# Kernel optimization log

Measured on AMD Instinct MI355X. Metric: run time of the kernel, lower is better.

The kernel has to match this reference:

```python
import jax, jax.numpy as jnp
import numpy as np

B, T, F, M = 32, 256, 512, 4   # batch, pred_len (=d_model=state_size), feature_dim (=mamba seq), time-mark feats
N = F - M                      # number of variates in x_enc
T2 = 2 * T
EPS = 1e-5


def setup_inputs() -> dict:
    key = jax.random.key(0)
    it = iter(jax.random.split(key, 32))
    def nrm(*s):
        return jax.random.normal(next(it), s, jnp.float32) * 0.02
    inp = {
        "x_enc": jax.random.normal(next(it), (B, T, N), jnp.float32),
        "x_mark_enc": jax.random.normal(next(it), (B, T, M), jnp.float32),
        "x_dec": jnp.zeros((1, 1, 1), jnp.float32),
        "x_mark_dec": jnp.zeros((1, 1, 1), jnp.float32),
        # 3 structurally identical MambaBlocks -> stack params on leading dim 3
        "norm_w": jnp.ones((3, T), jnp.float32),
        "inp_W": nrm(3, T, T2), "inp_b": jnp.zeros((3, T2), jnp.float32),
        "conv_W": nrm(3, F, F, 3), "conv_b": jnp.zeros((3, F), jnp.float32),
        "convlin_W": nrm(3, T2, T2), "convlin_b": jnp.zeros((3, T2), jnp.float32),
        "fc1_W": nrm(3, T2, T2), "fc1_b": jnp.zeros((3, T2), jnp.float32),
        "fc2_W": nrm(3, T2, T), "fc2_b": jnp.zeros((3, T), jnp.float32),
        "fc3_W": nrm(3, T2, T), "fc3_b": jnp.zeros((3, T), jnp.float32),
        "D_W": nrm(3, T, T2), "D_b": jnp.zeros((3, T2), jnp.float32),
        "out_W": nrm(3, T2, T), "out_b": jnp.ones((3, T), jnp.float32),  # out_proj.bias init to 1.0
        "proj_W": nrm(T, T), "proj_b": jnp.zeros((T,), jnp.float32),
    }
    return inp


def _rmsnorm(x, w):
    return x * jax.lax.rsqrt(jnp.mean(x * x, -1, keepdims=True) + EPS) * w


def _conv1d(x, W, b):
    # x: [B, C, L], W: [C_out, C_in, 3], padding=1
    y = jax.lax.conv_general_dilated(x, W, (1,), [(1, 1)], dimension_numbers=("NCH", "OIH", "NCH"))
    return y + b[None, :, None]


def _s6(x, fc1W, fc1b, fc2W, fc2b, fc3W, fc3b):
    # h is zero-initialized each call, so dA=exp(delta*A) multiplies zeros and
    # y = einsum('bln,bldn->bld', C, x[...,None]*dB) = delta * x * <C,B>_n
    Bmat = x @ fc2W + fc2b                         # [B, L, n]
    Cmat = x @ fc3W + fc3b                         # [B, L, n]
    delta = jax.nn.softplus(x @ fc1W + fc1b)       # [B, L, d]
    cb = jnp.einsum("bln,bln->bl", Cmat, Bmat)   # contraction over state dim
    return delta * x * cb[:, :, None]


def _block(x, i, p):
    xn = _rmsnorm(x, p["norm_w"][i])
    xp = xn @ p["inp_W"][i] + p["inp_b"][i]                      # [B, F, 2T]
    xc = jax.nn.silu(_conv1d(xp, p["conv_W"][i], p["conv_b"][i]))
    xco = xc @ p["convlin_W"][i] + p["convlin_b"][i]
    xssm = _s6(xco, p["fc1_W"][i], p["fc1_b"][i], p["fc2_W"][i], p["fc2_b"][i], p["fc3_W"][i], p["fc3_b"][i])
    xres = jax.nn.silu(xn @ p["D_W"][i] + p["D_b"][i])
    return (jax.nn.silu(xssm) * xres) @ p["out_W"][i] + p["out_b"][i]


def _forward(x_enc, x_mark_enc, p):
    means = jax.lax.stop_gradient(jnp.mean(x_enc, 1, keepdims=True))  # detached in torch
    xe = x_enc - means
    stdev = jnp.sqrt(jnp.var(xe, axis=1, keepdims=True) + 1e-5)       # NOT detached in torch
    xe = xe / stdev
    x = jnp.concatenate([xe, x_mark_enc], axis=2).transpose(0, 2, 1)  # [B, F, T]
    for i in range(3):
        x = _block(x, i, p)
    dec = (x @ p["proj_W"] + p["proj_b"]).transpose(0, 2, 1)          # [B, T, F]
    return dec[:, :, :N] * stdev + means                              # pred_len == T


def reference(x_enc, x_mark_enc, x_dec, x_mark_dec, norm_w, inp_W, inp_b, conv_W, conv_b, convlin_W, convlin_b, fc1_W, fc1_b, fc2_W, fc2_b, fc3_W, fc3_b, D_W, D_b, out_W, out_b, proj_W, proj_b):
    p = dict(norm_w=norm_w, inp_W=inp_W, inp_b=inp_b, conv_W=conv_W, conv_b=conv_b, convlin_W=convlin_W, convlin_b=convlin_b, fc1_W=fc1_W, fc1_b=fc1_b, fc2_W=fc2_W, fc2_b=fc2_b, fc3_W=fc3_W, fc3_b=fc3_b, D_W=D_W, D_b=D_b, out_W=out_W, out_b=out_b, proj_W=proj_W, proj_b=proj_b)
    return _forward(x_enc, x_mark_enc, p)
```

## Files before the change

### kernel.cpp

```cpp
#include <hip/hip_runtime.h>
#include <hip/hip_bf16.h>
#include <math.h>

typedef __hip_bfloat16 bf16;
typedef short short8 __attribute__((ext_vector_type(8)));
typedef short short4v __attribute__((ext_vector_type(4)));
typedef float floatx4 __attribute__((ext_vector_type(4)));

constexpr int CB_ = 32;
constexpr int CT = 256;
constexpr int CF = 512;
constexpr int CN = 508;
constexpr int CM = 4;
constexpr int CT2 = 512;
constexpr int MROWS = CB_ * CF;
constexpr int PADL = 528;

__device__ __forceinline__ float b2f(bf16 v) { return __bfloat162float(v); }
__device__ __forceinline__ bf16 f2b(float v) { return __float2bfloat16(v); }
__device__ __forceinline__ float s2f(short s) {
    unsigned u = ((unsigned)(unsigned short)s) << 16;
    return __builtin_bit_cast(float, u);
}
__device__ __forceinline__ short f2s(float v) {
    bf16 t = __float2bfloat16(v);
    return __builtin_bit_cast(short, t);
}
__device__ __forceinline__ float silu_f(float x) { return x / (1.0f + __expf(-x)); }
__device__ __forceinline__ float softplus_f(float x) {
    return fmaxf(x, 0.0f) + __logf(1.0f + __expf(-fabsf(x)));
}

__device__ __forceinline__ void gl_lds16(const bf16* g, short* l) {
    __builtin_amdgcn_global_load_lds(
        (const __attribute__((address_space(1))) unsigned int*)(g),
        (__attribute__((address_space(3))) unsigned int*)(l), 16, 0, 0);
}


constexpr int CONV3 = 3 * 512 * 512;
constexpr int MTILES = 3520;
struct P8 { const float* s[8]; bf16* d[8]; };
__global__ __launch_bounds__(256) void prepack_all_kernel(P8 p, const float* __restrict__ nw,
                                                          const float* __restrict__ convW,
                                                          bf16* __restrict__ convD,
                                                          bf16* __restrict__ xpT,
                                                          float* __restrict__ CBv) {
    int bid = blockIdx.x;
    if (bid >= MTILES) {
        int idx = (bid - MTILES) * 256 + threadIdx.x;
        if (idx < CONV3) {
            int ci = idx & 511;
            int co = (idx >> 9) & 511;
            int ib = idx >> 18;
            const float* src = convW + ((size_t)(ib * 512 + co) * 512 + ci) * 3;
            #pragma unroll
            for (int t = 0; t < 3; t++)
                convD[(((size_t)(ib * 3 + t) * 512 + co) << 9) + ci] = f2b(src[t]);
        } else if (idx < CONV3 + 32768) {
            int j = idx - CONV3;
            int ci = j & 511;
            int w = (j >> 9) & 1;
            int b = j >> 10;
            xpT[((size_t)b * PADL + (w ? 513 : 0)) * 512 + ci] = f2b(0.0f);
        } else if (idx < CONV3 + 32768 + MROWS) {
            CBv[idx - CONV3 - 32768] = 0.0f;
        }
        return;
    }
    const int Ks[8]   = {256, 256, 512, 512, 512, 512, 512, 256};
    const int Ns[8]   = {512, 512, 512, 256, 256, 512, 256, 256};
    const int zs[8]   = {3, 3, 3, 3, 3, 3, 3, 1};
    const int dstr[8] = {262144, 262144, 524288, 524288, 524288, 262144, 131072, 65536};
    const int rml[8]  = {1, 1, 1, 2, 2, 1, 1, 1};
    const int rad[8]  = {0, 0, 0, 0, 1, 0, 0, 0};
    int m = 0, acc = 0;
    for (m = 0; m < 8; m++) {
        int c = (Ns[m] >> 5) * (Ks[m] >> 5) * zs[m];
        if (bid < acc + c) break;
        acc += c;
    }
    int lid = bid - acc;
    int K = Ks[m], N = Ns[m];
    int tx = N >> 5, ty = K >> 5;
    int z = lid / (tx * ty), rem = lid % (tx * ty);
    int k0 = (rem / tx) * 32, n0 = (rem % tx) * 32;
    const float* s = p.s[m] + (size_t)z * K * N;
    bf16* d = p.d[m] + (size_t)z * dstr[m];
    int mul = rml[m], add = rad[m];
    bool fold = (m <= 1);
    __shared__ float Ts[32][33];
    for (int e = threadIdx.x; e < 1024; e += 256) {
        int r = e >> 5, c = e & 31;
        float v = s[(size_t)(k0 + r) * N + n0 + c];
        if (fold) v *= nw[z * 256 + k0 + r];
        Ts[r][c] = v;
    }
    __syncthreads();
    for (int e = threadIdx.x; e < 1024; e += 256) {
        int r = e >> 5, c = e & 31;
        d[(size_t)((n0 + r) * mul + add) * K + k0 + c] = f2b(Ts[c][r]);
    }
}

__global__ __launch_bounds__(256) void buildx_kernel(
    const float* __restrict__ xe, const float* __restrict__ xm,
    float* __restrict__ means, float* __restrict__ stdev,
    bf16* __restrict__ X0, float* __restrict__ SCL) {
    __shared__ float L[256][65];
    __shared__ float red_s[4][64], red_q[4][64];
    __shared__ float stat_m[64], stat_i[64];
    int blk = blockIdx.x;
    int b = blk >> 3, f0 = (blk & 7) * 64;
    int tid = threadIdx.x;
    int j = tid & 63, tq = tid >> 6;
    int f = f0 + j;
    float ps = 0.f, pq = 0.f;
    const float* xep = xe + (size_t)b * CT * CN + f;
    const float* xmp = xm + (size_t)b * CT * CM + (f - CN);
    #pragma unroll 4
    for (int tt = 0; tt < 64; tt++) {
        int t = tq * 64 + tt;
        float v = (f < CN) ? xep[(size_t)t * CN] : xmp[(size_t)t * CM];
        L[t][j] = v;
        ps += v;
        pq += v * v;
    }
    red_s[tq][j] = ps;
    red_q[tq][j] = pq;
    __syncthreads();
    if (tid < 64) {
        int ff = f0 + tid;
        float s = red_s[0][tid] + red_s[1][tid] + red_s[2][tid] + red_s[3][tid];
        float q = red_q[0][tid] + red_q[1][tid] + red_q[2][tid] + red_q[3][tid];
        float mean, isd, msq;
        if (ff < CN) {
            mean = s * (1.0f / 256.0f);
            float var = fmaxf(q * (1.0f / 256.0f) - mean * mean, 0.0f);
            float sd = sqrtf(var + 1e-5f);
            isd = 1.0f / sd;
            means[b * CN + ff] = mean;
            stdev[b * CN + ff] = sd;
            msq = var / (var + 1e-5f);
        } else {
            mean = 0.0f;
            isd = 1.0f;
            msq = q * (1.0f / 256.0f);
        }
        stat_m[tid] = mean;
        stat_i[tid] = isd;
        SCL[b * 512 + ff] = rsqrtf(msq + 1e-5f);
    }
    __syncthreads();
    bf16* outp = X0 + ((size_t)(b * 512 + f0)) * 256;
    int t = tid;
    #pragma unroll 4
    for (int fp = 0; fp < 64; fp++) {
        float val = (L[t][fp] - stat_m[fp]) * stat_i[fp];
        outp[(size_t)fp * 256 + t] = f2b(val);
    }
}

template <int EPI>
__global__ __launch_bounds__(256) void g64_kernel(const bf16* __restrict__ A,
                                                  const bf16* __restrict__ Wt,
                                                  int K,
                                                  const float* __restrict__ b1,
                                                  const float* __restrict__ b2,
                                                  const float* __restrict__ SCL,
                                                  const float* __restrict__ CBin,
                                                  float* __restrict__ CBout,
                                                  bf16* __restrict__ o1,
                                                  bf16* __restrict__ o2,
                                                  int Ncols,
                                                  const float* __restrict__ means,
                                                  const float* __restrict__ stdev,
                                                  float* __restrict__ outf) {
    __shared__ __align__(16) short As[128 * 64];
    __shared__ __align__(16) short Bs[64 * 64];
    const int tid = threadIdx.x;
    const int lane = tid & 63;
    const int wave = tid >> 6;
    const int m0 = blockIdx.x * 128, n0 = blockIdx.y * 64;

    const int lrow8 = lane >> 3;
    const int lcolS = (((lane & 7) ^ lrow8) << 3);
    const int wm = (wave & 1) * 64, wn = (wave >> 1) * 32;
    const int fr = lane & 15, quad = lane >> 4;
    const int fr7 = fr & 7;

    floatx4 acc[4][2];
    #pragma unroll
    for (int i = 0; i < 4; i++)
        #pragma unroll
        for (int j = 0; j < 2; j++) acc[i][j] = (floatx4){0.f, 0.f, 0.f, 0.f};

    for (int k0 = 0; k0 < K; k0 += 64) {
        for (int ca = wave; ca < 16; ca += 4)
            gl_lds16(A + (size_t)(m0 + ca * 8 + lrow8) * K + k0 + lcolS, &As[ca * 512]);
        for (int cb = wave; cb < 8; cb += 4)
            gl_lds16(Wt + (size_t)(n0 + cb * 8 + lrow8) * K + k0 + lcolS, &Bs[cb * 512]);
        __syncthreads();
        #pragma unroll
        for (int s = 0; s < 2; s++) {
            const int co = (((s * 4 + quad) ^ fr7) << 3);
            short8 af[4], bfv[2];
            #pragma unroll
            for (int i = 0; i < 4; i++) af[i] = *(const short8*)&As[(wm + i * 16 + fr) * 64 + co];
            #pragma unroll
            for (int j = 0; j < 2; j++) bfv[j] = *(const short8*)&Bs[(wn + j * 16 + fr) * 64 + co];
            #pragma unroll
            for (int i = 0; i < 4; i++)
                #pragma unroll
                for (int j = 0; j < 2; j++)
                    acc[i][j] = __builtin_amdgcn_mfma_f32_16x16x32_bf16(af[i], bfv[j], acc[i][j], 0, 0, 0);
        }
        __syncthreads();
    }

    if (EPI == 0) {
        #pragma unroll
        for (int j = 0; j < 2; j++) {
            int n = n0 + wn + j * 16 + fr;
            float bv = b1[n];
            #pragma unroll
            for (int i = 0; i < 4; i++) {
                int mb = m0 + wm + i * 16 + quad * 4;
                #pragma unroll
                for (int r = 0; r < 4; r++)
                    o1[(size_t)(mb + r) * Ncols + n] = f2b(acc[i][j][r] + bv);
            }
        }
    } else if (EPI == 3) {
        #pragma unroll
        for (int j = 0; j < 2; j++) {
            int t = n0 + wn + j * 16 + fr;
            float bv = b1[t];
            #pragma unroll
            for (int i = 0; i < 4; i++) {
                int mb = m0 + wm + i * 16 + quad * 4;
                int b = mb >> 9;
                int nv = mb & 511;
                if (nv < CN) {
                    floatx4 o;
                    #pragma unroll
                    for (int r = 0; r < 4; r++) {
                        int sn = b * CN + nv + r;
                        o[r] = (acc[i][j][r] + bv) * stdev[sn] + means[sn];
                    }
                    *(floatx4*)(outf + ((size_t)(b * CT + t)) * CN + nv) = o;
                }
            }
        }
    } else if (EPI == 4) {
        if (n0 < 512) {
            int b = (m0 + wm) >> 9;
            #pragma unroll
            for (int i = 0; i < 4; i++) {
                int mb = m0 + wm + i * 16 + quad * 4;
                float sclr[4];
                #pragma unroll
                for (int r = 0; r < 4; r++) sclr[r] = SCL[mb + r];
                int ci = mb & 511;
                #pragma unroll
                for (int j = 0; j < 2; j++) {
                    int n = n0 + wn + j * 16 + fr;
                    float bv = b1[n];
                    bf16* dst = o1 + ((size_t)b * PADL + n + 1) * 512;
                    short4v pk;
                    #pragma unroll
                    for (int r = 0; r < 4; r++) pk[r] = f2s(acc[i][j][r] * sclr[r] + bv);
                    *(short4v*)(dst + ci) = pk;
                }
            }
        } else {
            #pragma unroll
            for (int i = 0; i < 4; i++) {
                int mb = m0 + wm + i * 16 + quad * 4;
                float sclr[4];
                #pragma unroll
                for (int r = 0; r < 4; r++) sclr[r] = SCL[mb + r];
                #pragma unroll
                for (int j = 0; j < 2; j++) {
                    int n = n0 + wn + j * 16 + fr;
                    float bv = b2[n - 512];
                    #pragma unroll
                    for (int r = 0; r < 4; r++)
                        o2[(size_t)(mb + r) * 512 + (n - 512)] =
                            f2b(silu_f(acc[i][j][r] * sclr[r] + bv));
                }
            }
        }
    } else if (EPI == 5) {
        if (n0 < 512) {
            #pragma unroll
            for (int i = 0; i < 4; i++) {
                int mb = m0 + wm + i * 16 + quad * 4;
                #pragma unroll
                for (int j = 0; j < 2; j++) {
                    int n = n0 + wn + j * 16 + fr;
                    float bv = b1[n];
                    #pragma unroll
                    for (int r = 0; r < 4; r++) {
                        size_t off = (size_t)(mb + r) * 512 + n;
                        float delta = softplus_f(acc[i][j][r] + bv);
                        outf[off] = delta * b2f(A[off]);
                    }
                }
            }
        } else {
            float bv[2];
            #pragma unroll
            for (int j = 0; j < 2; j++) {
                int nn = n0 + wn + j * 16 + fr - 512;
                int c = nn >> 1;
                bv[j] = (fr & 1) ? CBin[c] : b2[c];
            }
            #pragma unroll
            for (int i = 0; i < 4; i++) {
                #pragma unroll
                for (int r = 0; r < 4; r++) {
                    float s = 0.f;
                    #pragma unroll
                    for (int j = 0; j < 2; j++) {
                        float v = acc[i][j][r] + bv[j];
                        s += v * __shfl_xor(v, 1);
                    }
                    s += __shfl_xor(s, 2);
                    s += __shfl_xor(s, 4);
                    s += __shfl_xor(s, 8);
                    if (fr == 0)
                        atomicAdd(&CBout[m0 + wm + i * 16 + quad * 4 + r], s * 0.5f);
                }
            }
        }
    }
}

__global__ __launch_bounds__(256) void conv_mfma_kernel(const bf16* __restrict__ Wc,
                                                        const bf16* __restrict__ xpT,
                                                        const float* __restrict__ bias,
                                                        bf16* __restrict__ Out,
                                                        float* __restrict__ CBvZ) {
    __shared__ __align__(16) short As[3 * 64 * 64];
    __shared__ __align__(16) short Bs[72 * 64];
    const int tid = threadIdx.x;
    const int lane = tid & 63;
    const int wave = tid >> 6;
    int bx = blockIdx.x;
    if (bx < 128 && tid < 128) CBvZ[bx * 128 + tid] = 0.0f;
    int b = bx >> 6, rem = bx & 63;
    int mt = rem >> 3, nt = rem & 7;
    const int m0 = mt * 64, n0 = nt * 64;
    const bf16* xb = xpT + (size_t)b * PADL * 512;

    const int lrow8 = lane >> 3;
    const int lcolS = (((lane & 7) ^ lrow8) << 3);
    const int wm = (wave & 1) * 32, wn = (wave >> 1) * 32;
    const int fr = lane & 15, quad = lane >> 4;
    const int fr7 = fr & 7;

    floatx4 acc[2][2];
    #pragma unroll
    for (int i = 0; i < 2; i++)
        #pragma unroll
        for (int j = 0; j < 2; j++) acc[i][j] = (floatx4){0.f, 0.f, 0.f, 0.f};

    for (int k0 = 0; k0 < 512; k0 += 64) {
        for (int ga = wave; ga < 24; ga += 4) {
            int tap = ga >> 3, rg = ga & 7;
            gl_lds16(Wc + (size_t)tap * 262144 + (size_t)(m0 + rg * 8 + lrow8) * 512 + k0 + lcolS,
                     &As[tap * 4096 + rg * 512]);
        }
        for (int gb = wave; gb < 9; gb += 4) {
            gl_lds16(xb + (size_t)(n0 + gb * 8 + lrow8) * 512 + k0 + lcolS, &Bs[gb * 512]);
        }
        __syncthreads();
        #pragma unroll
        for (int s = 0; s < 2; s++) {
            const int sq = s * 4 + quad;
            #pragma unroll
            for (int tap = 0; tap < 3; tap++) {
                const int coA = ((sq ^ fr7) << 3);
                const int coB = ((sq ^ ((fr + tap) & 7)) << 3);
                short8 af[2], bfv[2];
                #pragma unroll
                for (int i = 0; i < 2; i++)
                    af[i] = *(const short8*)&As[tap * 4096 + (wm + i * 16 + fr) * 64 + coA];
                #pragma unroll
                for (int j = 0; j < 2; j++)
                    bfv[j] = *(const short8*)&Bs[(wn + j * 16 + fr + tap) * 64 + coB];
                #pragma unroll
                for (int i = 0; i < 2; i++)
                    #pragma unroll
                    for (int j = 0; j < 2; j++)
                        acc[i][j] = __builtin_amdgcn_mfma_f32_16x16x32_bf16(af[i], bfv[j], acc[i][j], 0, 0, 0);
            }
        }
        __syncthreads();
    }
    bf16* ob = Out + (size_t)b * CF * CT2;
    #pragma unroll
    for (int i = 0; i < 2; i++) {
        int mb = m0 + wm + i * 16 + quad * 4;
        #pragma unroll
        for (int r = 0; r < 4; r++) {
            float bv = bias[mb + r];
            #pragma unroll
            for (int j = 0; j < 2; j++) {
                int n = n0 + wn + j * 16 + fr;
                ob[(size_t)(mb + r) * CT2 + n] = f2b(silu_f(acc[i][j][r] + bv));
            }
        }
    }
}

__global__ __launch_bounds__(256) void gemm_scl_gate_kernel(const float* __restrict__ P,
                                                            const bf16* __restrict__ Xres,
                                                            const float* __restrict__ CBv,
                                                            const bf16* __restrict__ Wt,
                                                            const float* __restrict__ bias,
                                                            bf16* __restrict__ Xo,
                                                            float* __restrict__ SCL) {
    __shared__ __align__(16) short As[32 * 64];
    __shared__ __align__(16) short Bs[256 * 64];
    __shared__ float red[4][32];
    const int tid = threadIdx.x;
    const int lane = tid & 63;
    const int wave = tid >> 6;
    const int m0 = blockIdx.x * 32;

    const int lrow8 = lane >> 3;
    const int lcolS = (((lane & 7) ^ lrow8) << 3);
    const int wn = wave * 64;
    const int fr = lane & 15, quad = lane >> 4;
    const int fr7 = fr & 7;

    floatx4 acc[2][4];
    #pragma unroll
    for (int i = 0; i < 2; i++)
        #pragma unroll
        for (int j = 0; j < 4; j++) acc[i][j] = (floatx4){0.f, 0.f, 0.f, 0.f};

    const int arow = m0 + wave * 8 + lrow8;
    const float cbr = CBv[arow];

    for (int k0 = 0; k0 < 512; k0 += 64) {
        for (int c = wave; c < 32; c += 4)
            gl_lds16(Wt + (size_t)(c * 8 + lrow8) * 512 + k0 + lcolS, &Bs[c * 512]);
        {
            int col = k0 + lcolS;
            const float* pp = P + (size_t)arow * 512 + col;
            floatx4 p0 = *(const floatx4*)pp;
            floatx4 p1 = *(const floatx4*)(pp + 4);
            short8 xr = *(const short8*)(Xres + (size_t)arow * 512 + col);
            short8 g;
            #pragma unroll
            for (int e = 0; e < 4; e++) {
                g[e] = f2s(silu_f(p0[e] * cbr) * s2f(xr[e]));
                g[4 + e] = f2s(silu_f(p1[e] * cbr) * s2f(xr[4 + e]));
            }
            *(short8*)&As[wave * 512 + lrow8 * 64 + (lane & 7) * 8] = g;
        }
        __syncthreads();
        #pragma unroll
        for (int s = 0; s < 2; s++) {
            const int co = (((s * 4 + quad) ^ fr7) << 3);
            short8 af[2], bfv[4];
            #pragma unroll
            for (int i = 0; i < 2; i++) af[i] = *(const short8*)&As[(i * 16 + fr) * 64 + co];
            #pragma unroll
            for (int j = 0; j < 4; j++) bfv[j] = *(const short8*)&Bs[(wn + j * 16 + fr) * 64 + co];
            #pragma unroll
            for (int i = 0; i < 2; i++)
                #pragma unroll
                for (int j = 0; j < 4; j++)
                    acc[i][j] = __builtin_amdgcn_mfma_f32_16x16x32_bf16(af[i], bfv[j], acc[i][j], 0, 0, 0);
        }
        __syncthreads();
    }
    #pragma unroll
    for (int j = 0; j < 4; j++) {
        float bv = bias[wn + j * 16 + fr];
        #pragma unroll
        for (int i = 0; i < 2; i++)
            #pragma unroll
            for (int r = 0; r < 4; r++) acc[i][j][r] += bv;
    }
    #pragma unroll
    for (int i = 0; i < 2; i++) {
        #pragma unroll
        for (int r = 0; r < 4; r++) {
            float s = 0.f;
            #pragma unroll
            for (int j = 0; j < 4; j++) s += acc[i][j][r] * acc[i][j][r];
            #pragma unroll
            for (int o = 8; o > 0; o >>= 1) s += __shfl_xor(s, o);
            if (fr == 0) red[wave][i * 16 + quad * 4 + r] = s;
        }
    }
    __syncthreads();
    if (tid < 32) {
        float tot = red[0][tid] + red[1][tid] + red[2][tid] + red[3][tid];
        SCL[m0 + tid] = rsqrtf(tot * (1.0f / CT) + 1e-5f);
    }
    #pragma unroll
    for (int j = 0; j < 4; j++) {
        int n = wn + j * 16 + fr;
        #pragma unroll
        for (int i = 0; i < 2; i++) {
            int rl = i * 16 + quad * 4;
            #pragma unroll
            for (int r = 0; r < 4; r++)
                Xo[(size_t)(m0 + rl + r) * CT + n] = f2b(acc[i][j][r]);
        }
    }
}

extern "C" void kernel_launch(void* const* d_in, const int* in_sizes, int n_in,
                              void* d_out, int out_size, void* d_ws, size_t ws_size,
                              hipStream_t stream) {
    const float* x_enc  = (const float*)d_in[0];
    const float* x_mark = (const float*)d_in[1];
    const float* norm_w = (const float*)d_in[4];
    const float* inp_W  = (const float*)d_in[5];
    const float* inp_b  = (const float*)d_in[6];
    const float* conv_W = (const float*)d_in[7];
    const float* conv_b = (const float*)d_in[8];
    const float* convlin_W = (const float*)d_in[9];
    const float* convlin_b = (const float*)d_in[10];
    const float* fc1_W = (const float*)d_in[11];
    const float* fc1_b = (const float*)d_in[12];
    const float* fc2_W = (const float*)d_in[13];
    const float* fc2_b = (const float*)d_in[14];
    const float* fc3_W = (const float*)d_in[15];
    const float* fc3_b = (const float*)d_in[16];
    const float* D_W   = (const float*)d_in[17];
    const float* D_b   = (const float*)d_in[18];
    const float* out_W = (const float*)d_in[19];
    const float* out_b = (const float*)d_in[20];
    const float* proj_W = (const float*)d_in[21];
    const float* proj_b = (const float*)d_in[22];

    char* ws = (char*)d_ws;
    float* MEANS = (float*)(ws);
    float* STDEV = (float*)(ws + 65536);
    float* CBv   = (float*)(ws + 131072);
    float* SCL   = (float*)(ws + 196608);
    bf16* wt = (bf16*)(ws + 262144);
    bf16* wt_g1      = wt;
    bf16* wt_g3      = wt + 786432;
    bf16* wt_convlin = wt + 2359296;
    bf16* wt_out     = wt + 3145728;
    bf16* wt_proj    = wt + 3538944;
    bf16* wt_conv    = wt + 3604480;
    bf16* xpT = (bf16*)(ws + 12189696);
    const size_t POOLB = 16777216;
    bf16* X    = (bf16*)(ws + 29491200);
    bf16* XRES = (bf16*)(ws + 29491200 + POOLB);
    bf16* XC   = (bf16*)(ws + 29491200 + 2 * POOLB);
    bf16* XCO  = (bf16*)(ws + 29491200 + 3 * POOLB);
    float* Pf  = (float*)(ws + 29491200 + 4 * POOLB);
    float* out = (float*)d_out;

    P8 p;
    p.s[0] = inp_W;  p.d[0] = wt_g1;
    p.s[1] = D_W;    p.d[1] = wt_g1 + 131072;
    p.s[2] = fc1_W;  p.d[2] = wt_g3;
    p.s[3] = fc2_W;  p.d[3] = wt_g3 + 262144;
    p.s[4] = fc3_W;  p.d[4] = wt_g3 + 262144;
    p.s[5] = convlin_W; p.d[5] = wt_convlin;
    p.s[6] = out_W;  p.d[6] = wt_out;
    p.s[7] = proj_W; p.d[7] = wt_proj;
    int tailBlocks = (CONV3 + 32768 + MROWS + 255) / 256;
    prepack_all_kernel<<<MTILES + tailBlocks, 256, 0, stream>>>(
        p, norm_w, conv_W, wt_conv, xpT, CBv);

    buildx_kernel<<<256, 256, 0, stream>>>(x_enc, x_mark, MEANS, STDEV, X, SCL);

    for (int i = 0; i < 3; i++) {
        g64_kernel<4><<<dim3(128, 16), 256, 0, stream>>>(
            X, wt_g1 + (size_t)i * 262144, 256, inp_b + i * CT2, D_b + i * CT2, SCL,
            nullptr, nullptr, xpT, XRES, 1024, nullptr, nullptr, nullptr);
        conv_mfma_kernel<<<2048, 256, 0, stream>>>(wt_conv + (size_t)i * 786432, xpT,
                                                   conv_b + i * CF, XC, CBv);
        g64_kernel<0><<<dim3(128, 8), 256, 0, stream>>>(
            XC, wt_convlin + (size_t)i * 262144, 512, convlin_b + i * CT2, nullptr, nullptr,
            nullptr, nullptr, XCO, nullptr, 512, nullptr, nullptr, nullptr);
        g64_kernel<5><<<dim3(128, 16), 256, 0, stream>>>(
            XCO, wt_g3 + (size_t)i * 524288, 512, fc1_b + i * CT2, fc2_b + i * CT, nullptr,
            fc3_b + i * CT, CBv, nullptr, nullptr, 0, nullptr, nullptr, Pf);
        gemm_scl_gate_kernel<<<512, 256, 0, stream>>>(
            Pf, XRES, CBv, wt_out + (size_t)i * 131072, out_b + i * CT, X, SCL);
    }

    g64_kernel<3><<<dim3(128, 4), 256, 0, stream>>>(
        X, wt_proj, 256, proj_b, nullptr, nullptr, nullptr, nullptr, nullptr,
        nullptr, 0, MEANS, STDEV, out);
}
```

Before: 514.4 us.

## Store delta*x in bf16, split gate GEMM over N with atomic sum-of-squares

The fc1 epilogue now writes delta*x as bf16 instead of fp32, halving that intermediate's traffic. The gated out-projection GEMM is split into two column halves to double its block count. Because a block no longer sees a full row, the RMS statistic is accumulated as a sum of squares with atomicAdd, and consumers compute rsqrt on the fly. The SSQ buffer is zeroed inside the fc1 kernel, which adds atomics, a cross-kernel ordering dependency and an extra bf16 rounding of the intermediate.

```diff
diff --git a/kernel.cpp b/kernel.cpp
--- a/kernel.cpp
+++ b/kernel.cpp
@@ -106,7 +106,7 @@
 __global__ __launch_bounds__(256) void buildx_kernel(
     const float* __restrict__ xe, const float* __restrict__ xm,
     float* __restrict__ means, float* __restrict__ stdev,
-    bf16* __restrict__ X0, float* __restrict__ SCL) {
+    bf16* __restrict__ X0, float* __restrict__ SSQ) {
     __shared__ float L[256][65];
     __shared__ float red_s[4][64], red_q[4][64];
     __shared__ float stat_m[64], stat_i[64];
@@ -149,7 +149,7 @@
         }
         stat_m[tid] = mean;
         stat_i[tid] = isd;
-        SCL[b * 512 + ff] = rsqrtf(msq + 1e-5f);
+        SSQ[b * 512 + ff] = msq * 256.0f;
     }
     __syncthreads();
     bf16* outp = X0 + ((size_t)(b * 512 + f0)) * 256;
@@ -167,7 +167,7 @@
                                                   int K,
                                                   const float* __restrict__ b1,
                                                   const float* __restrict__ b2,
-                                                  const float* __restrict__ SCL,
+                                                  const float* __restrict__ SSQ,
                                                   const float* __restrict__ CBin,
                                                   float* __restrict__ CBout,
                                                   bf16* __restrict__ o1,
@@ -183,6 +183,8 @@
     const int wave = tid >> 6;
     const int m0 = blockIdx.x * 128, n0 = blockIdx.y * 64;
 
+    if (EPI == 5 && blockIdx.y == 0 && tid < 128) outf[blockIdx.x * 128 + tid] = 0.0f;
+
     const int lrow8 = lane >> 3;
     const int lcolS = (((lane & 7) ^ lrow8) << 3);
     const int wm = (wave & 1) * 64, wn = (wave >> 1) * 32;
@@ -260,7 +262,8 @@
                 int mb = m0 + wm + i * 16 + quad * 4;
                 float sclr[4];
                 #pragma unroll
-                for (int r = 0; r < 4; r++) sclr[r] = SCL[mb + r];
+                for (int r = 0; r < 4; r++)
+                    sclr[r] = rsqrtf(SSQ[mb + r] * (1.0f / 256.0f) + 1e-5f);
                 int ci = mb & 511;
                 #pragma unroll
                 for (int j = 0; j < 2; j++) {
@@ -279,7 +282,8 @@
                 int mb = m0 + wm + i * 16 + quad * 4;
                 float sclr[4];
                 #pragma unroll
-                for (int r = 0; r < 4; r++) sclr[r] = SCL[mb + r];
+                for (int r = 0; r < 4; r++)
+                    sclr[r] = rsqrtf(SSQ[mb + r] * (1.0f / 256.0f) + 1e-5f);
                 #pragma unroll
                 for (int j = 0; j < 2; j++) {
                     int n = n0 + wn + j * 16 + fr;
@@ -304,7 +308,7 @@
                     for (int r = 0; r < 4; r++) {
                         size_t off = (size_t)(mb + r) * 512 + n;
                         float delta = softplus_f(acc[i][j][r] + bv);
-                        outf[off] = delta * b2f(A[off]);
+                        o1[off] = f2b(delta * b2f(A[off]));
                     }
                 }
             }
@@ -415,73 +419,68 @@
     }
 }
 
-__global__ __launch_bounds__(256) void gemm_scl_gate_kernel(const float* __restrict__ P,
+__global__ __launch_bounds__(256) void gemm_scl_gate_kernel(const bf16* __restrict__ P,
                                                             const bf16* __restrict__ Xres,
                                                             const float* __restrict__ CBv,
                                                             const bf16* __restrict__ Wt,
                                                             const float* __restrict__ bias,
                                                             bf16* __restrict__ Xo,
-                                                            float* __restrict__ SCL) {
+                                                            float* __restrict__ SSQ) {
     __shared__ __align__(16) short As[32 * 64];
-    __shared__ __align__(16) short Bs[256 * 64];
-    __shared__ float red[4][32];
+    __shared__ __align__(16) short Bs[128 * 64];
     const int tid = threadIdx.x;
     const int lane = tid & 63;
     const int wave = tid >> 6;
-    const int m0 = blockIdx.x * 32;
+    const int m0 = blockIdx.x * 32, n0 = blockIdx.y * 128;
 
     const int lrow8 = lane >> 3;
     const int lcolS = (((lane & 7) ^ lrow8) << 3);
-    const int wn = wave * 64;
+    const int wn = wave * 32;
     const int fr = lane & 15, quad = lane >> 4;
     const int fr7 = fr & 7;
 
-    floatx4 acc[2][4];
+    floatx4 acc[2][2];
     #pragma unroll
     for (int i = 0; i < 2; i++)
         #pragma unroll
-        for (int j = 0; j < 4; j++) acc[i][j] = (floatx4){0.f, 0.f, 0.f, 0.f};
+        for (int j = 0; j < 2; j++) acc[i][j] = (floatx4){0.f, 0.f, 0.f, 0.f};
 
     const int arow = m0 + wave * 8 + lrow8;
     const float cbr = CBv[arow];
 
     for (int k0 = 0; k0 < 512; k0 += 64) {
-        for (int c = wave; c < 32; c += 4)
-            gl_lds16(Wt + (size_t)(c * 8 + lrow8) * 512 + k0 + lcolS, &Bs[c * 512]);
+        for (int c = wave; c < 16; c += 4)
+            gl_lds16(Wt + (size_t)(n0 + c * 8 + lrow8) * 512 + k0 + lcolS, &Bs[c * 512]);
         {
             int col = k0 + lcolS;
-            const float* pp = P + (size_t)arow * 512 + col;
-            floatx4 p0 = *(const floatx4*)pp;
-            floatx4 p1 = *(const floatx4*)(pp + 4);
+            short8 pv = *(const short8*)(P + (size_t)arow * 512 + col);
             short8 xr = *(const short8*)(Xres + (size_t)arow * 512 + col);
             short8 g;
             #pragma unroll
-            for (int e = 0; e < 4; e++) {
-                g[e] = f2s(silu_f(p0[e] * cbr) * s2f(xr[e]));
-                g[4 + e] = f2s(silu_f(p1[e] * cbr) * s2f(xr[4 + e]));
-            }
+            for (int e = 0; e < 8; e++)
+                g[e] = f2s(silu_f(s2f(pv[e]) * cbr) * s2f(xr[e]));
             *(short8*)&As[wave * 512 + lrow8 * 64 + (lane & 7) * 8] = g;
         }
         __syncthreads();
         #pragma unroll
         for (int s = 0; s < 2; s++) {
             const int co = (((s * 4 + quad) ^ fr7) << 3);
-            short8 af[2], bfv[4];
+            short8 af[2], bfv[2];
             #pragma unroll
             for (int i = 0; i < 2; i++) af[i] = *(const short8*)&As[(i * 16 + fr) * 64 + co];
             #pragma unroll
-            for (int j = 0; j < 4; j++) bfv[j] = *(const short8*)&Bs[(wn + j * 16 + fr) * 64 + co];
+            for (int j = 0; j < 2; j++) bfv[j] = *(const short8*)&Bs[(wn + j * 16 + fr) * 64 + co];
             #pragma unroll
             for (int i = 0; i < 2; i++)
                 #pragma unroll
-                for (int j = 0; j < 4; j++)
+                for (int j = 0; j < 2; j++)
                     acc[i][j] = __builtin_amdgcn_mfma_f32_16x16x32_bf16(af[i], bfv[j], acc[i][j], 0, 0, 0);
         }
         __syncthreads();
     }
     #pragma unroll
-    for (int j = 0; j < 4; j++) {
-        float bv = bias[wn + j * 16 + fr];
+    for (int j = 0; j < 2; j++) {
+        float bv = bias[n0 + wn + j * 16 + fr];
         #pragma unroll
         for (int i = 0; i < 2; i++)
             #pragma unroll
@@ -493,20 +492,15 @@
         for (int r = 0; r < 4; r++) {
             float s = 0.f;
             #pragma unroll
-            for (int j = 0; j < 4; j++) s += acc[i][j][r] * acc[i][j][r];
+            for (int j = 0; j < 2; j++) s += acc[i][j][r] * acc[i][j][r];
             #pragma unroll
             for (int o = 8; o > 0; o >>= 1) s += __shfl_xor(s, o);
-            if (fr == 0) red[wave][i * 16 + quad * 4 + r] = s;
-        }
-    }
-    __syncthreads();
-    if (tid < 32) {
-        float tot = red[0][tid] + red[1][tid] + red[2][tid] + red[3][tid];
-        SCL[m0 + tid] = rsqrtf(tot * (1.0f / CT) + 1e-5f);
-    }
-    #pragma unroll
-    for (int j = 0; j < 4; j++) {
-        int n = wn + j * 16 + fr;
+            if (fr == 0) atomicAdd(&SSQ[m0 + i * 16 + quad * 4 + r], s);
+        }
+    }
+    #pragma unroll
+    for (int j = 0; j < 2; j++) {
+        int n = n0 + wn + j * 16 + fr;
         #pragma unroll
         for (int i = 0; i < 2; i++) {
             int rl = i * 16 + quad * 4;
@@ -546,7 +540,7 @@
     float* MEANS = (float*)(ws);
     float* STDEV = (float*)(ws + 65536);
     float* CBv   = (float*)(ws + 131072);
-    float* SCL   = (float*)(ws + 196608);
+    float* SSQ   = (float*)(ws + 196608);
     bf16* wt = (bf16*)(ws + 262144);
     bf16* wt_g1      = wt;
     bf16* wt_g3      = wt + 786432;
@@ -560,7 +554,7 @@
     bf16* XRES = (bf16*)(ws + 29491200 + POOLB);
     bf16* XC   = (bf16*)(ws + 29491200 + 2 * POOLB);
     bf16* XCO  = (bf16*)(ws + 29491200 + 3 * POOLB);
-    float* Pf  = (float*)(ws + 29491200 + 4 * POOLB);
+    bf16* Pb   = (bf16*)(ws + 29491200 + 4 * POOLB);
     float* out = (float*)d_out;
 
     P8 p;
@@ -576,11 +570,11 @@
     prepack_all_kernel<<<MTILES + tailBlocks, 256, 0, stream>>>(
         p, norm_w, conv_W, wt_conv, xpT, CBv);
 
-    buildx_kernel<<<256, 256, 0, stream>>>(x_enc, x_mark, MEANS, STDEV, X, SCL);
+    buildx_kernel<<<256, 256, 0, stream>>>(x_enc, x_mark, MEANS, STDEV, X, SSQ);
 
     for (int i = 0; i < 3; i++) {
         g64_kernel<4><<<dim3(128, 16), 256, 0, stream>>>(
-            X, wt_g1 + (size_t)i * 262144, 256, inp_b + i * CT2, D_b + i * CT2, SCL,
+            X, wt_g1 + (size_t)i * 262144, 256, inp_b + i * CT2, D_b + i * CT2, SSQ,
             nullptr, nullptr, xpT, XRES, 1024, nullptr, nullptr, nullptr);
         conv_mfma_kernel<<<2048, 256, 0, stream>>>(wt_conv + (size_t)i * 786432, xpT,
                                                    conv_b + i * CF, XC, CBv);
@@ -589,9 +583,9 @@
             nullptr, nullptr, XCO, nullptr, 512, nullptr, nullptr, nullptr);
         g64_kernel<5><<<dim3(128, 16), 256, 0, stream>>>(
             XCO, wt_g3 + (size_t)i * 524288, 512, fc1_b + i * CT2, fc2_b + i * CT, nullptr,
-            fc3_b + i * CT, CBv, nullptr, nullptr, 0, nullptr, nullptr, Pf);
-        gemm_scl_gate_kernel<<<512, 256, 0, stream>>>(
-            Pf, XRES, CBv, wt_out + (size_t)i * 131072, out_b + i * CT, X, SCL);
+            fc3_b + i * CT, CBv, Pb, nullptr, 0, nullptr, nullptr, SSQ);
+        gemm_scl_gate_kernel<<<dim3(512, 2), 256, 0, stream>>>(
+            Pb, XRES, CBv, wt_out + (size_t)i * 131072, out_b + i * CT, X, SSQ);
     }
 
     g64_kernel<3><<<dim3(128, 4), 256, 0, stream>>>(
```

Result: slower. 549.3 us (+6.8%).

## Double-buffer g64 GEMM LDS tiles with BK=32 and async prefetch

Applied to the files above, without the earlier changes.

Rewrites the g64 GEMM main loop to use two LDS buffers with a K-tile of 32 instead of a single buffer with 64. The next tile's global-to-LDS loads are issued before computing the current one, with a manual vmcnt wait and sched barriers. The goal is to overlap global load latency with MFMA work. In exchange it drops the XOR swizzle, which may cause LDS bank conflicts, and it runs twice as many barrier pairs per K.

```diff
diff --git a/kernel.cpp b/kernel.cpp
--- a/kernel.cpp
+++ b/kernel.cpp
@@ -37,6 +37,8 @@
         (__attribute__((address_space(3))) unsigned int*)(l), 16, 0, 0);
 }
 
+
+#define PIPE_FENCE __builtin_amdgcn_sched_barrier(0)
 
 constexpr int CONV3 = 3 * 512 * 512;
 constexpr int MTILES = 3520;
@@ -176,18 +178,23 @@
                                                   const float* __restrict__ means,
                                                   const float* __restrict__ stdev,
                                                   float* __restrict__ outf) {
-    __shared__ __align__(16) short As[128 * 64];
-    __shared__ __align__(16) short Bs[64 * 64];
+    __shared__ __align__(16) short As[2][128 * 32];
+    __shared__ __align__(16) short Bs[2][64 * 32];
     const int tid = threadIdx.x;
     const int lane = tid & 63;
     const int wave = tid >> 6;
     const int m0 = blockIdx.x * 128, n0 = blockIdx.y * 64;
 
-    const int lrow8 = lane >> 3;
-    const int lcolS = (((lane & 7) ^ lrow8) << 3);
+    const int lrow = lane >> 2;
+    const int lcol = (lane & 3) * 8;
+    const bf16* aP0 = A + (size_t)(m0 + wave * 32 + lrow) * K + lcol;
+    const bf16* aP1 = A + (size_t)(m0 + wave * 32 + 16 + lrow) * K + lcol;
+    const bf16* bP0 = Wt + (size_t)(n0 + wave * 16 + lrow) * K + lcol;
+    const int aOff = wave * 1024;
+    const int bOff = wave * 512;
+
     const int wm = (wave & 1) * 64, wn = (wave >> 1) * 32;
     const int fr = lane & 15, quad = lane >> 4;
-    const int fr7 = fr & 7;
 
     floatx4 acc[4][2];
     #pragma unroll
@@ -195,28 +202,46 @@
         #pragma unroll
         for (int j = 0; j < 2; j++) acc[i][j] = (floatx4){0.f, 0.f, 0.f, 0.f};
 
-    for (int k0 = 0; k0 < K; k0 += 64) {
-        for (int ca = wave; ca < 16; ca += 4)
-            gl_lds16(A + (size_t)(m0 + ca * 8 + lrow8) * K + k0 + lcolS, &As[ca * 512]);
-        for (int cb = wave; cb < 8; cb += 4)
-            gl_lds16(Wt + (size_t)(n0 + cb * 8 + lrow8) * K + k0 + lcolS, &Bs[cb * 512]);
-        __syncthreads();
-        #pragma unroll
-        for (int s = 0; s < 2; s++) {
-            const int co = (((s * 4 + quad) ^ fr7) << 3);
-            short8 af[4], bfv[2];
-            #pragma unroll
-            for (int i = 0; i < 4; i++) af[i] = *(const short8*)&As[(wm + i * 16 + fr) * 64 + co];
-            #pragma unroll
-            for (int j = 0; j < 2; j++) bfv[j] = *(const short8*)&Bs[(wn + j * 16 + fr) * 64 + co];
-            #pragma unroll
-            for (int i = 0; i < 4; i++)
-                #pragma unroll
-                for (int j = 0; j < 2; j++)
-                    acc[i][j] = __builtin_amdgcn_mfma_f32_16x16x32_bf16(af[i], bfv[j], acc[i][j], 0, 0, 0);
-        }
-        __syncthreads();
-    }
+    auto STAGE = [&](int buf, int k0) {
+        gl_lds16(aP0 + k0, &As[buf][aOff]);
+        gl_lds16(aP1 + k0, &As[buf][aOff + 512]);
+        gl_lds16(bP0 + k0, &Bs[buf][bOff]);
+    };
+    auto COMPUTE = [&](int buf) {
+        short8 af[4], bfv[2];
+        #pragma unroll
+        for (int i = 0; i < 4; i++)
+            af[i] = *(const short8*)&As[buf][(wm + i * 16 + fr) * 32 + quad * 8];
+        #pragma unroll
+        for (int j = 0; j < 2; j++)
+            bfv[j] = *(const short8*)&Bs[buf][(wn + j * 16 + fr) * 32 + quad * 8];
+        #pragma unroll
+        for (int i = 0; i < 4; i++)
+            #pragma unroll
+            for (int j = 0; j < 2; j++)
+                acc[i][j] = __builtin_amdgcn_mfma_f32_16x16x32_bf16(af[i], bfv[j], acc[i][j], 0, 0, 0);
+    };
+
+    STAGE(0, 0);
+    int cur = 0;
+    for (int k0 = 32; k0 < K; k0 += 32) {
+        STAGE(cur ^ 1, k0);
+        PIPE_FENCE;
+        asm volatile("s_waitcnt vmcnt(3)" ::: "memory");
+        PIPE_FENCE;
+        __builtin_amdgcn_s_barrier();
+        PIPE_FENCE;
+        COMPUTE(cur);
+        PIPE_FENCE;
+        __builtin_amdgcn_s_barrier();
+        cur ^= 1;
+    }
+    PIPE_FENCE;
+    asm volatile("s_waitcnt vmcnt(0)" ::: "memory");
+    PIPE_FENCE;
+    __builtin_amdgcn_s_barrier();
+    PIPE_FENCE;
+    COMPUTE(cur);
 
     if (EPI == 0) {
         #pragma unroll
```

Result: slower. 548.5 us (+6.6%).
